# Optimization experiments

Measured on AMD Instinct MI355X. Metric: run time of the kernel, lower is better.

The kernel has to match this reference:

```python
import jax, jax.numpy as jnp
import numpy as np

N_NODES = 100000
N_EDGES = 3200000
IN_DIM, HID_DIM, OUT_DIM = 256, 64, 32


def setup_inputs() -> dict:
    key = jax.random.key(0)
    ks = jax.random.split(key, 12)
    s = 0.05
    x = jax.random.normal(ks[0], (N_NODES, IN_DIM), dtype=jnp.float32)
    edge_index = jax.random.randint(ks[1], (2, N_EDGES), 0, N_NODES, dtype=jnp.int64)
    return {
        "x": x,
        "edge_index": edge_index,
        # GCNConv 1: in->hid
        "W1": jax.random.normal(ks[2], (IN_DIM, HID_DIM), dtype=jnp.float32) * s,
        "b1": jnp.zeros((HID_DIM,), dtype=jnp.float32),
        # GCNConv 2: hid->out
        "W2": jax.random.normal(ks[3], (HID_DIM, OUT_DIM), dtype=jnp.float32) * s,
        "b2": jnp.zeros((OUT_DIM,), dtype=jnp.float32),
        # weight_predictor MLP: Linear(out,hid) -> ReLU -> Linear(hid,1) -> Sigmoid
        "Wp1": jax.random.normal(ks[4], (OUT_DIM, HID_DIM), dtype=jnp.float32) * s,
        "bp1": jnp.zeros((HID_DIM,), dtype=jnp.float32),
        "Wp2": jax.random.normal(ks[5], (HID_DIM, 1), dtype=jnp.float32) * s,
        "bp2": jnp.zeros((1,), dtype=jnp.float32),
    }


def gcn_conv(h, src, dst, deg_norm, W, b, n_nodes):
    """PyG GCNConv: x' = D^-1/2 (A+I) D^-1/2 (x W) + b, edges incl. self-loops."""
    h = h @ W                                   # [N, F_out]
    coef = deg_norm[src] * deg_norm[dst]        # [E+N]
    agg = jax.ops.segment_sum(h[src] * coef[:, None], dst, num_segments=n_nodes)
    return agg + b


def reference(x, edge_index, W1, b1, W2, b2, Wp1, bp1, Wp2, bp2):
    n = x.shape[0]
    loop = jnp.arange(n, dtype=edge_index.dtype)
    src = jnp.concatenate([edge_index[0], loop])  # self-loops appended
    dst = jnp.concatenate([edge_index[1], loop])
    # degree (with self-loops) on target nodes, deg^-1/2 with inf->0
    deg = jax.ops.segment_sum(jnp.ones_like(dst, dtype=x.dtype), dst, num_segments=n)
    deg_norm = jnp.where(deg > 0, jax.lax.rsqrt(deg), 0.0)

    h = gcn_conv(x, src, dst, deg_norm, W1, b1, n)
    h = jax.nn.relu(h)                            # dropout inactive (eval)
    h = gcn_conv(h, src, dst, deg_norm, W2, b2, n)  # no relu after last conv

    # weight predictor MLP head
    p = jax.nn.relu(h @ Wp1 + bp1)
    node_weights = jax.nn.sigmoid(p @ Wp2 + bp2)  # [N, 1]
    return h, node_weights
```

## Files before the change

kernel.cpp:

```cpp
#include <hip/hip_runtime.h>
#include <hip/hip_fp16.h>
#include <cstdint>
#include <cstddef>

#define N_NODES 100000
#define N_EDGES 3200000
#define IN_DIM  256
#define HID_DIM 64
#define OUT_DIM 32

#define NBINS      391
#define BIN_SHIFT  8
#define BIN_STRIDE 9216
#define BIN_EPB    8192

typedef unsigned int uint;
typedef unsigned char uchar;
typedef unsigned short ushort;

__device__ __forceinline__ float2 h2tof2(uint u) {
    __half2 h = *reinterpret_cast<const __half2*>(&u);
    return __half22float2(h);
}
__device__ __forceinline__ uint f2toh2(float a, float b) {
    __half2 h = __floats2half2_rn(a, b);
    return *reinterpret_cast<const uint*>(&h);
}
__device__ __forceinline__ ushort f2h(float a) {
    __half h = __float2half_rn(a);
    return *reinterpret_cast<const ushort*>(&h);
}
__device__ __forceinline__ void fma_mix_lo(float& acc, float w, uint v) {
    asm("v_fma_mix_f32 %0, %1, %2, %0 op_sel:[0,0,0] op_sel_hi:[0,1,0]"
        : "+v"(acc) : "v"(w), "v"(v));
}
__device__ __forceinline__ void fma_mix_hi(float& acc, float w, uint v) {
    asm("v_fma_mix_f32 %0, %1, %2, %0 op_sel:[0,1,0] op_sel_hi:[0,1,0]"
        : "+v"(acc) : "v"(w), "v"(v));
}

__global__ __launch_bounds__(512)
void k_bin(const int* __restrict__ ei, int* __restrict__ bin_cursor,
           uint* __restrict__ binned, int* __restrict__ bin_base,
           int* __restrict__ rowptr) {
    __shared__ int   lcount[NBINS];
    __shared__ int   lstart[NBINS];
    __shared__ int   lplace[NBINS];
    __shared__ int   gbase[NBINS];
    __shared__ int   sc[512];
    __shared__ uint  stage[BIN_EPB];
    __shared__ uchar binid[BIN_EPB];

    const int tid  = threadIdx.x;
    const int bid  = blockIdx.x;
    int*      done = bin_cursor + NBINS;

    const int e0   = bid * BIN_EPB;
    const int nval = min(BIN_EPB, N_EDGES - e0);

    for (int i = tid; i < NBINS; i += 512) lcount[i] = 0;
    __syncthreads();

    #pragma unroll
    for (int k = 0; k < BIN_EPB / 512; k += 4) {
        int d4[4];
        #pragma unroll
        for (int u = 0; u < 4; ++u) {
            int e = e0 + (k + u) * 512 + tid;
            d4[u] = (e < N_EDGES) ? ei[N_EDGES + e] : -1;
        }
        #pragma unroll
        for (int u = 0; u < 4; ++u)
            if (d4[u] >= 0) atomicAdd(&lcount[d4[u] >> BIN_SHIFT], 1);
    }
    __syncthreads();

    int v = (tid < NBINS) ? lcount[tid] : 0;
    sc[tid] = v; __syncthreads();
    for (int off = 1; off < 512; off <<= 1) {
        int x = sc[tid];
        if (tid >= off) x += sc[tid - off];
        __syncthreads(); sc[tid] = x; __syncthreads();
    }
    if (tid < NBINS) {
        int excl = sc[tid] - v;
        lstart[tid] = excl;
        lplace[tid] = excl;
        gbase[tid]  = atomicAdd(&bin_cursor[tid], v);
    }
    __syncthreads();

    #pragma unroll
    for (int k = 0; k < BIN_EPB / 512; k += 4) {
        int s4[4], d4[4];
        #pragma unroll
        for (int u = 0; u < 4; ++u) {
            int e = e0 + (k + u) * 512 + tid;
            bool ok = (e < N_EDGES);
            s4[u] = ok ? ei[e] : -1;
            d4[u] = ok ? ei[N_EDGES + e] : 0;
        }
        #pragma unroll
        for (int u = 0; u < 4; ++u) {
            if (s4[u] >= 0) {
                int b = d4[u] >> BIN_SHIFT;
                int p = atomicAdd(&lplace[b], 1);
                stage[p] = (uint)s4[u] | ((uint)(d4[u] & 255) << 17)
                         | ((uint)(b >> 8) << 25);
                binid[p] = (uchar)(b & 255);
            }
        }
    }
    __syncthreads();

    for (int i = tid; i < nval; i += 512) {
        uint ed = stage[i];
        int  b  = (int)binid[i] | (int)((ed >> 25) & 1u) << 8;
        int  gix = gbase[b] + (i - lstart[b]);
        if (gix < BIN_STRIDE)
            binned[(size_t)b * BIN_STRIDE + gix] = ed;
    }
    __syncthreads();

    if (tid == 0) {
        __threadfence();
        lcount[0] = (atomicAdd(done, 1) == gridDim.x - 1) ? 1 : 0;
    }
    __syncthreads();
    if (lcount[0]) {
        int t = tid;
        int vv = 0;
        if (t < NBINS) vv = min(atomicAdd(&bin_cursor[t], 0), BIN_STRIDE);
        sc[t] = vv; __syncthreads();
        for (int off = 1; off < 512; off <<= 1) {
            int x = sc[t];
            if (t >= off) x += sc[t - off];
            __syncthreads(); sc[t] = x; __syncthreads();
        }
        if (t < NBINS)      bin_base[t] = sc[t] - vv;
        if (t == NBINS - 1) rowptr[N_NODES] = sc[t];
    }
}

__global__ __launch_bounds__(512)
void k_csr(const uint* __restrict__ binned, const int* __restrict__ bin_cursor,
           const int* __restrict__ bin_base, int* __restrict__ rowptr,
           float* __restrict__ dn, int* __restrict__ csr) {
    __shared__ int lcnt[256];
    __shared__ int lpl[256];
    __shared__ int sc[256];
    __shared__ int csr_s[BIN_STRIDE];

    const int tid   = threadIdx.x;
    const int b     = blockIdx.x;
    const int n0    = b << BIN_SHIFT;
    const int cnt   = min(bin_cursor[b], BIN_STRIDE);
    const int ebase = bin_base[b];
    const uint* bb  = binned + (size_t)b * BIN_STRIDE;

    if (tid < 256) lcnt[tid] = 0;
    __syncthreads();

    for (int i0 = tid; i0 < cnt; i0 += 2048) {
        uint e4[4]; int ok[4];
        #pragma unroll
        for (int u = 0; u < 4; ++u) {
            int i = i0 + u * 512;
            ok[u] = (i < cnt);
            e4[u] = bb[ok[u] ? i : 0];
        }
        #pragma unroll
        for (int u = 0; u < 4; ++u)
            if (ok[u]) atomicAdd(&lcnt[(e4[u] >> 17) & 255u], 1);
    }
    __syncthreads();

    int v = 0;
    if (tid < 256) { v = lcnt[tid]; sc[tid] = v; }
    __syncthreads();
    for (int off = 1; off < 256; off <<= 1) {
        int x = 0;
        if (tid < 256) { x = sc[tid]; if (tid >= off) x += sc[tid - off]; }
        __syncthreads();
        if (tid < 256) sc[tid] = x;
        __syncthreads();
    }
    if (tid < 256) {
        int excl = sc[tid] - v;
        lpl[tid] = excl;
        int n = n0 + tid;
        if (n < N_NODES) {
            rowptr[n] = ebase + excl;
            dn[n]     = rsqrtf((float)v + 1.0f);
        }
    }
    __syncthreads();

    for (int i0 = tid; i0 < cnt; i0 += 2048) {
        uint e4[4]; int ok[4];
        #pragma unroll
        for (int u = 0; u < 4; ++u) {
            int i = i0 + u * 512;
            ok[u] = (i < cnt);
            e4[u] = bb[ok[u] ? i : 0];
        }
        #pragma unroll
        for (int u = 0; u < 4; ++u) {
            if (ok[u]) {
                int p = atomicAdd(&lpl[(e4[u] >> 17) & 255u], 1);
                csr_s[p] = (int)(e4[u] & 0x1FFFFu);
            }
        }
    }
    __syncthreads();
    for (int i = tid; i < cnt; i += 512)
        csr[ebase + i] = csr_s[i];
}

template<int KD, int NC>
__global__ __launch_bounds__(32 * (NC / 8))
void k_gemm_h(const float* __restrict__ X, const float* __restrict__ W,
              uint* __restrict__ Yh, int M) {
    constexpr int TC = NC / 8;
    constexpr int THREADS = 32 * TC;
    constexpr int KC = 32;
    __shared__ float Xs[128][33];
    __shared__ float Ws[KC][NC];

    const int tid  = threadIdx.x;
    const int tr   = tid / TC;
    const int tc   = tid % TC;
    const int row0 = blockIdx.x * 128;

    float acc[4][8];
    #pragma unroll
    for (int i = 0; i < 4; ++i)
        #pragma unroll
        for (int j = 0; j < 8; ++j) acc[i][j] = 0.f;

    for (int kc = 0; kc < KD; kc += KC) {
        #pragma unroll
        for (int i = tid; i < 128 * (KC / 4); i += THREADS) {
            int r  = i / (KC / 4);
            int k4 = (i % (KC / 4)) * 4;
            float4 v = make_float4(0.f, 0.f, 0.f, 0.f);
            int gr = row0 + r;
            if (gr < M)
                v = *reinterpret_cast<const float4*>(&X[(size_t)gr * KD + kc + k4]);
            Xs[r][k4 + 0] = v.x; Xs[r][k4 + 1] = v.y;
            Xs[r][k4 + 2] = v.z; Xs[r][k4 + 3] = v.w;
        }
        #pragma unroll
        for (int i = tid; i < KC * (NC / 4); i += THREADS) {
            int kk = i / (NC / 4);
            int c4 = (i % (NC / 4)) * 4;
            *reinterpret_cast<float4*>(&Ws[kk][c4]) =
                *reinterpret_cast<const float4*>(&W[(size_t)(kc + kk) * NC + c4]);
        }
        __syncthreads();

        #pragma unroll
        for (int kk = 0; kk < KC; ++kk) {
            float xv[4];
            #pragma unroll
            for (int i = 0; i < 4; ++i) xv[i] = Xs[tr * 4 + i][kk];
            float4 w0 = *reinterpret_cast<const float4*>(&Ws[kk][tc * 8]);
            float4 w1 = *reinterpret_cast<const float4*>(&Ws[kk][tc * 8 + 4]);
            float wv[8] = {w0.x, w0.y, w0.z, w0.w, w1.x, w1.y, w1.z, w1.w};
            #pragma unroll
            for (int i = 0; i < 4; ++i)
                #pragma unroll
                for (int j = 0; j < 8; ++j)
                    acc[i][j] = fmaf(xv[i], wv[j], acc[i][j]);
        }
        __syncthreads();
    }

    #pragma unroll
    for (int i = 0; i < 4; ++i) {
        int gr = row0 + tr * 4 + i;
        if (gr < M) {
            uint4 o;
            o.x = f2toh2(acc[i][0], acc[i][1]);
            o.y = f2toh2(acc[i][2], acc[i][3]);
            o.z = f2toh2(acc[i][4], acc[i][5]);
            o.w = f2toh2(acc[i][6], acc[i][7]);
            *reinterpret_cast<uint4*>(&Yh[(size_t)gr * (NC / 2) + tc * 4]) = o;
        }
    }
}

__global__ __launch_bounds__(256)
void k_agg1(const uint* __restrict__ H1h, const int* __restrict__ rowptr,
            const int* __restrict__ csr, const float* __restrict__ dn,
            const float* __restrict__ b1, const float* __restrict__ W2,
            ushort* __restrict__ H2h) {
    __shared__ float W2s[HID_DIM * OUT_DIM];
    for (int i = threadIdx.x; i < HID_DIM * OUT_DIM; i += 256) W2s[i] = W2[i];
    __syncthreads();

    int wid  = (blockIdx.x * blockDim.x + threadIdx.x) >> 6;
    int lane = threadIdx.x & 63;
    if (wid >= N_NODES / 2) return;
    const int half = lane >> 5;
    const int hb   = half << 5;
    const int l    = lane & 31;
    const int n    = 2 * wid + half;

    int rp = (l < 2) ? rowptr[n + l] : 0;
    int base = __shfl(rp, hb + 0);
    int cnt  = __shfl(rp, hb + 1) - base;
    const float dnn = dn[n];

    float2 self2 = h2tof2(H1h[(size_t)n * 32 + l]);
    float2 acc;
    acc.x = dnn * self2.x;
    acc.y = dnn * self2.y;

    const int cnt2 = max(cnt, __shfl_xor(cnt, 32));
    for (int b0 = 0; b0 < cnt2; b0 += 32) {
        int m_own = min(32, cnt - b0);
        int m_max = min(32, cnt2 - b0);
        int s = 0; float dsv = 0.f;
        if (l < m_own) { s = csr[base + b0 + l]; dsv = dn[s]; }
        for (int j0 = 0; j0 < m_max; j0 += 8) {
            uint v[8]; float w[8];
            #pragma unroll
            for (int i = 0; i < 8; ++i) {
                int j  = j0 + i;
                int sj = __shfl(s, hb + j);
                w[i] = __shfl(dsv, hb + j);
                v[i] = H1h[(size_t)sj * 32 + l];
            }
            #pragma unroll
            for (int i = 0; i < 8; ++i) {
                fma_mix_lo(acc.x, w[i], v[i]);
                fma_mix_hi(acc.y, w[i], v[i]);
            }
        }
    }
    float2 b1q = *reinterpret_cast<const float2*>(b1 + 2 * l);
    float2 o;
    o.x = fmaxf(b1q.x + dnn * acc.x, 0.f);
    o.y = fmaxf(b1q.y + dnn * acc.y, 0.f);

    const int c = lane & 31, hh = lane >> 5;
    #pragma unroll
    for (int nodesel = 0; nodesel < 2; ++nodesel) {
        const int nb = nodesel << 5;
        float acc2 = 0.f;
        #pragma unroll
        for (int fi = 0; fi < 32; ++fi) {
            int f = hh * 32 + fi;
            float vv = (f & 1) ? __shfl(o.y, nb + (f >> 1))
                               : __shfl(o.x, nb + (f >> 1));
            acc2 = fmaf(vv, W2s[f * OUT_DIM + c], acc2);
        }
        acc2 += __shfl_xor(acc2, 32);
        if (hh == 0) H2h[(size_t)(2 * wid + nodesel) * 32 + c] = f2h(acc2);
    }
}

__global__ __launch_bounds__(256)
void k_agg2m(const uint* __restrict__ H2h, const int* __restrict__ rowptr,
             const int* __restrict__ csr, const float* __restrict__ dn,
             const float* __restrict__ b2, const float* __restrict__ Wp1,
             const float* __restrict__ bp1, const float* __restrict__ Wp2,
             const float* __restrict__ bp2, float* __restrict__ out_h,
             float* __restrict__ out_w) {
    __shared__ float Wp1s[OUT_DIM * HID_DIM];
    __shared__ float Wp2s[HID_DIM];
    __shared__ float bp1s[HID_DIM];
    for (int i = threadIdx.x; i < OUT_DIM * HID_DIM; i += 256) Wp1s[i] = Wp1[i];
    if (threadIdx.x < HID_DIM) {
        Wp2s[threadIdx.x] = Wp2[threadIdx.x];
        bp1s[threadIdx.x] = bp1[threadIdx.x];
    }
    __syncthreads();

    int wid  = (blockIdx.x * blockDim.x + threadIdx.x) >> 6;
    int lane = threadIdx.x & 63;
    if (wid >= N_NODES / 2) return;
    const int nd  = lane >> 5;
    const int nb0 = nd << 5;
    const int l32 = lane & 31;
    const int l   = lane & 15;
    const int h2  = (lane >> 4) & 1;
    const int n   = 2 * wid + nd;

    int rp = (lane < 3) ? rowptr[2 * wid + lane] : 0;
    int base = __shfl(rp, nd);
    int cnt  = __shfl(rp, nd + 1) - base;
    const float dnn = dn[n];

    float2 self2 = h2tof2(H2h[(size_t)n * 16 + l]);
    float2 acc;
    acc.x = (h2 == 0) ? dnn * self2.x : 0.f;
    acc.y = (h2 == 0) ? dnn * self2.y : 0.f;

    const int cnt2 = max(cnt, __shfl_xor(cnt, 32));
    for (int b0 = 0; b0 < cnt2; b0 += 32) {
        int m_own = min(32, cnt - b0);
        int m_max = min(32, cnt2 - b0);
        int s = 0; float dsv = 0.f;
        if (l32 < m_own) { s = csr[base + b0 + l32]; dsv = dn[s]; }
        for (int j0 = h2; j0 < m_max; j0 += 16) {
            uint v[8]; float w[8];
            #pragma unroll
            for (int i = 0; i < 8; ++i) {
                int j  = j0 + 2 * i;
                int sj = __shfl(s, nb0 + j);
                w[i] = __shfl(dsv, nb0 + j);
                v[i] = H2h[(size_t)sj * 16 + l];
            }
            #pragma unroll
            for (int i = 0; i < 8; ++i) {
                fma_mix_lo(acc.x, w[i], v[i]);
                fma_mix_hi(acc.y, w[i], v[i]);
            }
        }
    }
    acc.x += __shfl_xor(acc.x, 16);
    acc.y += __shfl_xor(acc.y, 16);
    float2 b2q = *reinterpret_cast<const float2*>(b2 + 2 * l);
    float2 hv;
    hv.x = b2q.x + dnn * acc.x;
    hv.y = b2q.y + dnn * acc.y;
    if (h2 == 0)
        *reinterpret_cast<float2*>(out_h + (size_t)n * OUT_DIM + 2 * l) = hv;

    #pragma unroll
    for (int nodesel = 0; nodesel < 2; ++nodesel) {
        const int nb = nodesel << 5;
        float p = bp1s[lane];
        #pragma unroll
        for (int ff = 0; ff < OUT_DIM; ++ff) {
            float hf = (ff & 1) ? __shfl(hv.y, nb + (ff >> 1))
                                : __shfl(hv.x, nb + (ff >> 1));
            p = fmaf(hf, Wp1s[ff * HID_DIM + lane], p);
        }
        p = fmaxf(p, 0.f);
        float z = p * Wp2s[lane];
        #pragma unroll
        for (int off = 32; off; off >>= 1) z += __shfl_xor(z, off);
        if (lane == 0)
            out_w[2 * wid + nodesel] = 1.f / (1.f + __expf(-(z + bp2[0])));
    }
}

extern "C" void kernel_launch(void* const* d_in, const int* in_sizes, int n_in,
                              void* d_out, int out_size, void* d_ws, size_t ws_size,
                              hipStream_t stream) {
    const float* x   = (const float*)d_in[0];
    const int*   ei  = (const int*)d_in[1];
    const float* W1  = (const float*)d_in[2];
    const float* b1  = (const float*)d_in[3];
    const float* W2  = (const float*)d_in[4];
    const float* b2  = (const float*)d_in[5];
    const float* Wp1 = (const float*)d_in[6];
    const float* bp1 = (const float*)d_in[7];
    const float* Wp2 = (const float*)d_in[8];
    const float* bp2 = (const float*)d_in[9];
    float* out = (float*)d_out;

    char* ws = (char*)d_ws;
    int*    bin_cursor = (int*)   (ws + 0);
    int*    bin_base   = (int*)   (ws + 2048);
    int*    rowptr     = (int*)   (ws + 4096);
    float*  dn         = (float*) (ws + 404480);
    int*    csr        = (int*)   (ws + 804608);
    uint*   binned     = (uint*)  (ws + 13604608);
    uint*   H1h        = (uint*)  (ws + 28018432);
    ushort* H2h        = (ushort*)(ws + 40818432);

    hipMemsetAsync(bin_cursor, 0, (NBINS + 1) * sizeof(int), stream);

    k_bin<<<(N_EDGES + BIN_EPB - 1) / BIN_EPB, 512, 0, stream>>>(ei, bin_cursor, binned,
                                                                 bin_base, rowptr);
    k_csr<<<NBINS, 512, 0, stream>>>(binned, bin_cursor, bin_base, rowptr, dn, csr);
    k_gemm_h<IN_DIM, HID_DIM><<<(N_NODES + 127) / 128, 256, 0, stream>>>(x, W1, H1h, N_NODES);

    k_agg1<<<(N_NODES / 2 + 3) / 4, 256, 0, stream>>>(H1h, rowptr, csr, dn, b1, W2, H2h);
    k_agg2m<<<(N_NODES / 2 + 3) / 4, 256, 0, stream>>>((const uint*)H2h, rowptr, csr, dn, b2,
                                                       Wp1, bp1, Wp2, bp2,
                                                       out, out + (size_t)N_NODES * OUT_DIM);
}
```

Measured before the change: 278.6 us.

## Partition CSR rows by source-node chunk and sweep chunks in persistent layer-1 aggregation

The CSR build now sorts each destination row's neighbours into four source-range chunks and stores four row pointers per node. The first aggregation kernel becomes persistent: each wave handles up to seven node pairs and walks all of them chunk by chunk. The goal is that, at any moment, all waves gather H1 rows from roughly the same quarter of the node table, which improves cache locality. The cost is more registers for the seven accumulators, a larger rowptr array, extra key arithmetic (a division) in CSR construction, and possible load imbalance across waves.

Result: slower. 347.5 us (+24.7%).

```diff
diff --git a/kernel.cpp b/kernel.cpp
--- a/kernel.cpp
+++ b/kernel.cpp
@@ -14,6 +14,13 @@
 #define BIN_STRIDE 9216
 #define BIN_EPB    8192
 
+#define NCHUNK     4
+#define CHUNK_DIV  25000
+#define AGG_BLOCKS 2048
+#define AGG_WAVES  (AGG_BLOCKS * 4)
+#define PAIRS      (N_NODES / 2)
+#define KMAX       7
+
 typedef unsigned int uint;
 typedef unsigned char uchar;
 typedef unsigned short ushort;
@@ -42,7 +49,7 @@
 __global__ __launch_bounds__(512)
 void k_bin(const int* __restrict__ ei, int* __restrict__ bin_cursor,
            uint* __restrict__ binned, int* __restrict__ bin_base,
-           int* __restrict__ rowptr) {
+           int* __restrict__ rowptr2) {
     __shared__ int   lcount[NBINS];
     __shared__ int   lstart[NBINS];
     __shared__ int   lplace[NBINS];
@@ -138,17 +145,17 @@
             __syncthreads(); sc[t] = x; __syncthreads();
         }
         if (t < NBINS)      bin_base[t] = sc[t] - vv;
-        if (t == NBINS - 1) rowptr[N_NODES] = sc[t];
+        if (t == NBINS - 1) rowptr2[NCHUNK * N_NODES] = sc[t];
     }
 }
 
 __global__ __launch_bounds__(512)
 void k_csr(const uint* __restrict__ binned, const int* __restrict__ bin_cursor,
-           const int* __restrict__ bin_base, int* __restrict__ rowptr,
+           const int* __restrict__ bin_base, int* __restrict__ rowptr2,
            float* __restrict__ dn, int* __restrict__ csr) {
-    __shared__ int lcnt[256];
-    __shared__ int lpl[256];
-    __shared__ int sc[256];
+    __shared__ int lcnt[1024];
+    __shared__ int lpl[1024];
+    __shared__ int sc2[512];
     __shared__ int csr_s[BIN_STRIDE];
 
     const int tid   = threadIdx.x;
@@ -158,7 +165,7 @@
     const int ebase = bin_base[b];
     const uint* bb  = binned + (size_t)b * BIN_STRIDE;
 
-    if (tid < 256) lcnt[tid] = 0;
+    lcnt[tid] = 0; lcnt[tid + 512] = 0;
     __syncthreads();
 
     for (int i0 = tid; i0 < cnt; i0 += 2048) {
@@ -170,28 +177,42 @@
             e4[u] = bb[ok[u] ? i : 0];
         }
         #pragma unroll
-        for (int u = 0; u < 4; ++u)
-            if (ok[u]) atomicAdd(&lcnt[(e4[u] >> 17) & 255u], 1);
-    }
-    __syncthreads();
-
-    int v = 0;
-    if (tid < 256) { v = lcnt[tid]; sc[tid] = v; }
-    __syncthreads();
-    for (int off = 1; off < 256; off <<= 1) {
-        int x = 0;
-        if (tid < 256) { x = sc[tid]; if (tid >= off) x += sc[tid - off]; }
-        __syncthreads();
-        if (tid < 256) sc[tid] = x;
-        __syncthreads();
-    }
+        for (int u = 0; u < 4; ++u) {
+            if (ok[u]) {
+                int key = (int)((e4[u] >> 17) & 255u) * NCHUNK
+                        + (int)(e4[u] & 0x1FFFFu) / CHUNK_DIV;
+                atomicAdd(&lcnt[key], 1);
+            }
+        }
+    }
+    __syncthreads();
+
     if (tid < 256) {
-        int excl = sc[tid] - v;
-        lpl[tid] = excl;
         int n = n0 + tid;
         if (n < N_NODES) {
-            rowptr[n] = ebase + excl;
-            dn[n]     = rsqrtf((float)v + 1.0f);
+            int vt = lcnt[4 * tid] + lcnt[4 * tid + 1]
+                   + lcnt[4 * tid + 2] + lcnt[4 * tid + 3];
+            dn[n] = rsqrtf((float)vt + 1.0f);
+        }
+    }
+
+    int a0 = lcnt[2 * tid], a1 = lcnt[2 * tid + 1];
+    int s  = a0 + a1;
+    sc2[tid] = s; __syncthreads();
+    for (int off = 1; off < 512; off <<= 1) {
+        int x = sc2[tid];
+        if (tid >= off) x += sc2[tid - off];
+        __syncthreads(); sc2[tid] = x; __syncthreads();
+    }
+    int pair_excl = sc2[tid] - s;
+    lpl[2 * tid]     = pair_excl;
+    lpl[2 * tid + 1] = pair_excl + a0;
+    {
+        int key0 = 2 * tid;
+        int nl0  = key0 >> 2;
+        if (n0 + nl0 < N_NODES) {
+            rowptr2[4 * n0 + key0]     = ebase + pair_excl;
+            rowptr2[4 * n0 + key0 + 1] = ebase + pair_excl + a0;
         }
     }
     __syncthreads();
@@ -207,8 +228,10 @@
         #pragma unroll
         for (int u = 0; u < 4; ++u) {
             if (ok[u]) {
-                int p = atomicAdd(&lpl[(e4[u] >> 17) & 255u], 1);
-                csr_s[p] = (int)(e4[u] & 0x1FFFFu);
+                int src = (int)(e4[u] & 0x1FFFFu);
+                int key = (int)((e4[u] >> 17) & 255u) * NCHUNK + src / CHUNK_DIV;
+                int p = atomicAdd(&lpl[key], 1);
+                csr_s[p] = src;
             }
         }
     }
@@ -291,7 +314,7 @@
 }
 
 __global__ __launch_bounds__(256)
-void k_agg1(const uint* __restrict__ H1h, const int* __restrict__ rowptr,
+void k_agg1(const uint* __restrict__ H1h, const int* __restrict__ rowptr2,
             const int* __restrict__ csr, const float* __restrict__ dn,
             const float* __restrict__ b1, const float* __restrict__ W2,
             ushort* __restrict__ H2h) {
@@ -299,70 +322,91 @@
     for (int i = threadIdx.x; i < HID_DIM * OUT_DIM; i += 256) W2s[i] = W2[i];
     __syncthreads();
 
-    int wid  = (blockIdx.x * blockDim.x + threadIdx.x) >> 6;
-    int lane = threadIdx.x & 63;
-    if (wid >= N_NODES / 2) return;
-    const int half = lane >> 5;
-    const int hb   = half << 5;
-    const int l    = lane & 31;
-    const int n    = 2 * wid + half;
-
-    int rp = (l < 2) ? rowptr[n + l] : 0;
-    int base = __shfl(rp, hb + 0);
-    int cnt  = __shfl(rp, hb + 1) - base;
-    const float dnn = dn[n];
-
-    float2 self2 = h2tof2(H1h[(size_t)n * 32 + l]);
-    float2 acc;
-    acc.x = dnn * self2.x;
-    acc.y = dnn * self2.y;
-
-    const int cnt2 = max(cnt, __shfl_xor(cnt, 32));
-    for (int b0 = 0; b0 < cnt2; b0 += 32) {
-        int m_own = min(32, cnt - b0);
-        int m_max = min(32, cnt2 - b0);
-        int s = 0; float dsv = 0.f;
-        if (l < m_own) { s = csr[base + b0 + l]; dsv = dn[s]; }
-        for (int j0 = 0; j0 < m_max; j0 += 8) {
-            uint v[8]; float w[8];
+    const int wave0 = (blockIdx.x * 256 + threadIdx.x) >> 6;
+    const int lane  = threadIdx.x & 63;
+    const int half  = lane >> 5;
+    const int hb    = half << 5;
+    const int l     = lane & 31;
+
+    float2 acc[KMAX];
+    #pragma unroll
+    for (int k = 0; k < KMAX; ++k) {
+        acc[k] = make_float2(0.f, 0.f);
+        int pair = wave0 + k * AGG_WAVES;
+        if (pair < PAIRS) {
+            int n = 2 * pair + half;
+            float dnn = dn[n];
+            float2 s2 = h2tof2(H1h[(size_t)n * 32 + l]);
+            acc[k].x = dnn * s2.x;
+            acc[k].y = dnn * s2.y;
+        }
+    }
+
+    for (int c = 0; c < NCHUNK; ++c) {
+        #pragma unroll
+        for (int k = 0; k < KMAX; ++k) {
+            int pair = wave0 + k * AGG_WAVES;
+            if (pair >= PAIRS) continue;
+            int n = 2 * pair + half;
+            int rp = (l < 2) ? rowptr2[4 * n + c + l] : 0;
+            int base = __shfl(rp, hb + 0);
+            int cnt  = __shfl(rp, hb + 1) - base;
+            int cnt2 = max(cnt, __shfl_xor(cnt, 32));
+            for (int b0 = 0; b0 < cnt2; b0 += 32) {
+                int m_own = min(32, cnt - b0);
+                int m_max = min(32, cnt2 - b0);
+                int s = 0; float dsv = 0.f;
+                if (l < m_own) { s = csr[base + b0 + l]; dsv = dn[s]; }
+                for (int j0 = 0; j0 < m_max; j0 += 8) {
+                    uint v[8]; float w[8];
+                    #pragma unroll
+                    for (int i = 0; i < 8; ++i) {
+                        int j  = j0 + i;
+                        int sj = __shfl(s, hb + j);
+                        w[i] = __shfl(dsv, hb + j);
+                        v[i] = H1h[(size_t)sj * 32 + l];
+                    }
+                    #pragma unroll
+                    for (int i = 0; i < 8; ++i) {
+                        fma_mix_lo(acc[k].x, w[i], v[i]);
+                        fma_mix_hi(acc[k].y, w[i], v[i]);
+                    }
+                }
+            }
+        }
+    }
+
+    const int c2 = lane & 31, hh = lane >> 5;
+    #pragma unroll
+    for (int k = 0; k < KMAX; ++k) {
+        int pair = wave0 + k * AGG_WAVES;
+        if (pair >= PAIRS) continue;
+        int n = 2 * pair + half;
+        float dnn = dn[n];
+        float2 b1q = *reinterpret_cast<const float2*>(b1 + 2 * l);
+        float2 o;
+        o.x = fmaxf(b1q.x + dnn * acc[k].x, 0.f);
+        o.y = fmaxf(b1q.y + dnn * acc[k].y, 0.f);
+
+        #pragma unroll
+        for (int nodesel = 0; nodesel < 2; ++nodesel) {
+            const int nb = nodesel << 5;
+            float acc2 = 0.f;
             #pragma unroll
-            for (int i = 0; i < 8; ++i) {
-                int j  = j0 + i;
-                int sj = __shfl(s, hb + j);
-                w[i] = __shfl(dsv, hb + j);
-                v[i] = H1h[(size_t)sj * 32 + l];
-            }
-            #pragma unroll
-            for (int i = 0; i < 8; ++i) {
-                fma_mix_lo(acc.x, w[i], v[i]);
-                fma_mix_hi(acc.y, w[i], v[i]);
-            }
-        }
-    }
-    float2 b1q = *reinterpret_cast<const float2*>(b1 + 2 * l);
-    float2 o;
-    o.x = fmaxf(b1q.x + dnn * acc.x, 0.f);
-    o.y = fmaxf(b1q.y + dnn * acc.y, 0.f);
-
-    const int c = lane & 31, hh = lane >> 5;
-    #pragma unroll
-    for (int nodesel = 0; nodesel < 2; ++nodesel) {
-        const int nb = nodesel << 5;
-        float acc2 = 0.f;
-        #pragma unroll
-        for (int fi = 0; fi < 32; ++fi) {
-            int f = hh * 32 + fi;
-            float vv = (f & 1) ? __shfl(o.y, nb + (f >> 1))
-                               : __shfl(o.x, nb + (f >> 1));
-            acc2 = fmaf(vv, W2s[f * OUT_DIM + c], acc2);
-        }
-        acc2 += __shfl_xor(acc2, 32);
-        if (hh == 0) H2h[(size_t)(2 * wid + nodesel) * 32 + c] = f2h(acc2);
+            for (int fi = 0; fi < 32; ++fi) {
+                int f = hh * 32 + fi;
+                float vv = (f & 1) ? __shfl(o.y, nb + (f >> 1))
+                                   : __shfl(o.x, nb + (f >> 1));
+                acc2 = fmaf(vv, W2s[f * OUT_DIM + c2], acc2);
+            }
+            acc2 += __shfl_xor(acc2, 32);
+            if (hh == 0) H2h[(size_t)(2 * pair + nodesel) * 32 + c2] = f2h(acc2);
+        }
     }
 }
 
 __global__ __launch_bounds__(256)
-void k_agg2m(const uint* __restrict__ H2h, const int* __restrict__ rowptr,
+void k_agg2m(const uint* __restrict__ H2h, const int* __restrict__ rowptr2,
              const int* __restrict__ csr, const float* __restrict__ dn,
              const float* __restrict__ b2, const float* __restrict__ Wp1,
              const float* __restrict__ bp1, const float* __restrict__ Wp2,
@@ -388,7 +432,7 @@
     const int h2  = (lane >> 4) & 1;
     const int n   = 2 * wid + nd;
 
-    int rp = (lane < 3) ? rowptr[2 * wid + lane] : 0;
+    int rp = (lane < 3) ? rowptr2[8 * wid + 4 * lane] : 0;
     int base = __shfl(rp, nd);
     int cnt  = __shfl(rp, nd + 1) - base;
     const float dnn = dn[n];
@@ -466,22 +510,22 @@
     char* ws = (char*)d_ws;
     int*    bin_cursor = (int*)   (ws + 0);
     int*    bin_base   = (int*)   (ws + 2048);
-    int*    rowptr     = (int*)   (ws + 4096);
-    float*  dn         = (float*) (ws + 404480);
-    int*    csr        = (int*)   (ws + 804608);
-    uint*   binned     = (uint*)  (ws + 13604608);
-    uint*   H1h        = (uint*)  (ws + 28018432);
-    ushort* H2h        = (ushort*)(ws + 40818432);
+    int*    rowptr2    = (int*)   (ws + 4096);
+    float*  dn         = (float*) (ws + 1604608);
+    int*    csr        = (int*)   (ws + 2004608);
+    uint*   binned     = (uint*)  (ws + 14804608);
+    uint*   H1h        = (uint*)  (ws + 29218432);
+    ushort* H2h        = (ushort*)(ws + 42018432);
 
     hipMemsetAsync(bin_cursor, 0, (NBINS + 1) * sizeof(int), stream);
 
     k_bin<<<(N_EDGES + BIN_EPB - 1) / BIN_EPB, 512, 0, stream>>>(ei, bin_cursor, binned,
-                                                                 bin_base, rowptr);
-    k_csr<<<NBINS, 512, 0, stream>>>(binned, bin_cursor, bin_base, rowptr, dn, csr);
+                                                                 bin_base, rowptr2);
+    k_csr<<<NBINS, 512, 0, stream>>>(binned, bin_cursor, bin_base, rowptr2, dn, csr);
     k_gemm_h<IN_DIM, HID_DIM><<<(N_NODES + 127) / 128, 256, 0, stream>>>(x, W1, H1h, N_NODES);
 
-    k_agg1<<<(N_NODES / 2 + 3) / 4, 256, 0, stream>>>(H1h, rowptr, csr, dn, b1, W2, H2h);
-    k_agg2m<<<(N_NODES / 2 + 3) / 4, 256, 0, stream>>>((const uint*)H2h, rowptr, csr, dn, b2,
+    k_agg1<<<AGG_BLOCKS, 256, 0, stream>>>(H1h, rowptr2, csr, dn, b1, W2, (ushort*)H2h);
+    k_agg2m<<<(N_NODES / 2 + 3) / 4, 256, 0, stream>>>((const uint*)H2h, rowptr2, csr, dn, b2,
                                                        Wp1, bp1, Wp2, bp2,
                                                        out, out + (size_t)N_NODES * OUT_DIM);
 }
```
